# Kernel optimization log

Measured on AMD Instinct MI355X. Metric: run time of the kernel, lower is better.

The kernel has to match this reference:

```python
import jax, jax.numpy as jnp
import numpy as np

# Dimensions
B_, T_, IN_ = 8, 1024, 512          # batch, seq_len, in_dim
D_ = 1024                           # latent_dim (hidden_size)
I_ = 2048                           # intermediate_size
N_ = 64                             # state_size
H_ = 16                             # ssm_num_head
P_ = I_ // H_                       # head_dim = 128
K_ = 3                              # conv_kernel
L_ = 4                              # num_layer
OUT_, CB_ = 512, 1024               # out_dim, num_code_book
CONV_DIM = I_ + 2 * N_              # 2176
PROJ = I_ + CONV_DIM + H_           # in_proj width of mixer = 4240


def setup_inputs() -> dict:
    key = jax.random.key(0)
    ks = jax.random.split(key, 16)
    s = 0.02
    inp = {
        "x": jax.random.normal(ks[0], (B_, T_, IN_), jnp.float32),
        "in_w": jax.random.normal(ks[1], (IN_, D_), jnp.float32) * s,
        "in_b": jnp.zeros((D_,), jnp.float32),
        "norm_w": jnp.ones((L_, D_), jnp.float32),
        "mix_in_w": jax.random.normal(ks[2], (L_, D_, PROJ), jnp.float32) * s,
        "conv_w": jax.random.normal(ks[3], (L_, K_, 1, CONV_DIM), jnp.float32) * s,
        "conv_b": jnp.zeros((L_, CONV_DIM), jnp.float32),
        "dt_bias": jax.random.normal(ks[4], (L_, H_), jnp.float32) * 0.1,
        "A_log": jnp.log(jax.random.uniform(ks[5], (L_, H_), jnp.float32, 0.001, 0.1)),
        "D": jnp.ones((L_, H_), jnp.float32),
        "gnorm_w": jnp.ones((L_, I_), jnp.float32),
        "mix_out_w": jax.random.normal(ks[6], (L_, I_, D_), jnp.float32) * s,
        "out_w": jax.random.normal(ks[7], (D_, OUT_), jnp.float32) * s,
        "out_b": jnp.zeros((OUT_,), jnp.float32),
        "code_w": jax.random.normal(ks[8], (D_, CB_), jnp.float32) * s,
        "code_b": jnp.zeros((CB_,), jnp.float32),
    }
    return inp


def rmsnorm(x, w, eps=1e-6):
    v = jnp.mean(jnp.square(x), axis=-1, keepdims=True)
    return x * jax.lax.rsqrt(v + eps) * w


def mamba_block(x, nw, inw, cw, cb, dtb, alog, Dv, gnw, outw):
    residual = x
    h = rmsnorm(x, nw)
    proj = h @ inw                                   # [B,T,PROJ]
    gate, hBC, dt = jnp.split(proj, [I_, I_ + CONV_DIM], axis=-1)
    # causal depthwise conv along time
    conv = jax.lax.conv_general_dilated(
        hBC, cw, window_strides=(1,), padding=[(K_ - 1, 0)],
        dimension_numbers=("NWC", "WIO", "NWC"), feature_group_count=CONV_DIM)
    conv = jax.nn.silu(conv + cb)
    xs, Bm, Cm = jnp.split(conv, [I_, I_ + N_], axis=-1)   # [B,T,I],[B,T,N],[B,T,N]
    dt = jax.nn.softplus(dt + dtb)                   # [B,T,H]
    a = -jnp.exp(alog)                               # [H] scalar decay per head
    xh = xs.reshape(B_, T_, H_, P_)

    def step(hst, inp):
        dt_t, B_t, C_t, x_t = inp                    # [B,H],[B,N],[B,N],[B,H,P]
        dA = jnp.exp(dt_t * a)                       # [B,H]
        hst = hst * dA[:, :, None, None] + (dt_t[:, :, None, None] * x_t[..., None]) * B_t[:, None, None, :]
        y = jnp.einsum("bhpn,bn->bhp", hst, C_t)
        return hst, y

    inputs = (dt.transpose(1, 0, 2), Bm.transpose(1, 0, 2),
              Cm.transpose(1, 0, 2), xh.transpose(1, 0, 2, 3))
    h0 = jnp.zeros((B_, H_, P_, N_), x.dtype)
    _, ys = jax.lax.scan(step, h0, inputs)           # ys: [T,B,H,P]
    y = ys.transpose(1, 0, 2, 3) + Dv[None, None, :, None] * xh
    y = y.reshape(B_, T_, I_)
    y = rmsnorm(y * jax.nn.silu(gate), gnw)          # gated RMSNorm
    return residual + y @ outw


def reference(x, in_w, in_b, norm_w, mix_in_w, conv_w, conv_b, dt_bias,
              A_log, D, gnorm_w, mix_out_w, out_w, out_b, code_w, code_b):
    h = x @ in_w + in_b
    for i in range(L_):
        h = mamba_block(h, norm_w[i], mix_in_w[i], conv_w[i], conv_b[i],
                        dt_bias[i], A_log[i], D[i], gnorm_w[i], mix_out_w[i])
    return (h @ out_w + out_b, h @ code_w + code_b)
```

## Files before the change

kernel.cpp:

```cpp
#include <hip/hip_runtime.h>
#include <hip/hip_bf16.h>

typedef __hip_bfloat16 bf16;
typedef __bf16 bfv8 __attribute__((ext_vector_type(8)));
typedef float fv4 __attribute__((ext_vector_type(4)));

#define B_  8
#define T_  1024
#define INP 512
#define D_  1024
#define I_  2048
#define N_  64
#define H_  16
#define P_  128
#define L_  4
#define OUT_ 512
#define CB_ 1024
#define CONV_DIM 2176
#define PROJ 4240
#define M_  (B_*T_)
#define TC  64
#define NC  (T_/TC)

typedef const __attribute__((address_space(1))) void gv_t;
typedef __attribute__((address_space(3))) void lv_t;

__device__ __forceinline__ void load_lds16(const bf16* g, char* l) {
    __builtin_amdgcn_global_load_lds((gv_t*)g, (lv_t*)l, 16, 0, 0);
}

template <int N> __device__ __forceinline__ void wait_vm() {
    if constexpr (N == 0)      asm volatile("s_waitcnt vmcnt(0)" ::: "memory");
    else if constexpr (N == 2) asm volatile("s_waitcnt vmcnt(2)" ::: "memory");
    else if constexpr (N == 3) asm volatile("s_waitcnt vmcnt(3)" ::: "memory");
    else if constexpr (N == 4) asm volatile("s_waitcnt vmcnt(4)" ::: "memory");
    else if constexpr (N == 6) asm volatile("s_waitcnt vmcnt(6)" ::: "memory");
    else                       asm volatile("s_waitcnt vmcnt(8)" ::: "memory");
}
__device__ __forceinline__ void barrier_sync() {
    asm volatile("s_barrier" ::: "memory");
}

__global__ __launch_bounds__(256) void ingest_k(const float* __restrict__ src,
                                                bf16* __restrict__ dst, int n) {
    int i = blockIdx.x * 256 + threadIdx.x;
    if (i >= n) return;
    dst[i] = __float2bfloat16(src[i]);
}

__global__ __launch_bounds__(256) void transpose_any(const float* __restrict__ in,
                                                     size_t off,
                                                     bf16* __restrict__ out,
                                                     int R, int C) {
    __shared__ bf16 tile[32][33];
    int c0 = blockIdx.x * 32, r0 = blockIdx.y * 32;
    int tx = threadIdx.x, ty = threadIdx.y;
#pragma unroll
    for (int i = 0; i < 4; ++i) {
        int r = r0 + ty + i * 8, c = c0 + tx;
        bf16 v = __float2bfloat16(0.f);
        if (c < C) v = __float2bfloat16(in[off + (size_t)r * C + c]);
        tile[ty + i * 8][tx] = v;
    }
    __syncthreads();
#pragma unroll
    for (int i = 0; i < 4; ++i) {
        int c = c0 + ty + i * 8;
        out[(size_t)c * R + r0 + tx] = tile[tx][ty + i * 8];
    }
}

template <int MODE, int BM, int BN, int WGM, int WGN, int RING, int NTHR>
__global__ __launch_bounds__(NTHR) void gemm8p(const bf16* __restrict__ A,
                                               const bf16* __restrict__ Bt,
                                               int K, int N,
                                               const bf16* __restrict__ bias,
                                               float* __restrict__ outF,
                                               bf16* __restrict__ outB,
                                               bf16* __restrict__ outB2,
                                               float* __restrict__ outF2) {
    constexpr int HK = 32;
    constexpr int MT = BM / WGM / 16;
    constexpr int NT = BN / WGN / 16;
    constexpr int ABY = BM * HK * 2;
    constexpr int BBY = BN * HK * 2;
    constexpr int BUF = ABY + BBY;
    constexpr int RPI = NTHR / 4;
    constexpr int AL = BM / RPI;
    constexpr int BL = BN / RPI;
    constexpr int LD = AL + BL;
    constexpr int IB = NTHR * 16;

    extern __shared__ char lds[];
    const int tid = threadIdx.x;
    const int wv = tid >> 6, lane = tid & 63;
    const int l16 = lane & 15, quad = lane >> 4;
    const int wm = (wv / WGN) * (BM / WGM);
    const int wn = (wv % WGN) * (BN / WGN);

    const int NX = gridDim.x;
    const int nwg = NX * gridDim.y;
    const int orig = blockIdx.y * NX + blockIdx.x;
    const int q = nwg >> 3, r = nwg & 7, xcd = orig & 7, lid = orig >> 3;
    const int wg = (xcd < r ? xcd * (q + 1) : r * (q + 1) + (xcd - r) * q) + lid;
    const int m0 = (wg / NX) * BM;
    const int n0 = (wg % NX) * BN;

    const int srow = tid >> 2, sslot = tid & 3;
    const int swz = (sslot ^ ((srow >> 1) & 3)) << 3;
    const bf16* ga = A  + (size_t)(m0 + srow) * K + swz;
    const bf16* gb = Bt + (size_t)(n0 + srow) * K + swz;
    char* lw = lds + wv * 1024;

    const int HT = K / HK;

    auto stageA = [&](int stg, int rbuf) {
#pragma unroll
        for (int j = 0; j < AL; ++j)
            load_lds16(ga + (size_t)stg * HK + (size_t)(j * RPI) * K,
                       lw + rbuf * BUF + j * IB);
    };
    auto stageB = [&](int stg, int rbuf) {
#pragma unroll
        for (int j = 0; j < BL; ++j)
            load_lds16(gb + (size_t)stg * HK + (size_t)(j * RPI) * K,
                       lw + rbuf * BUF + ABY + j * IB);
    };

#pragma unroll
    for (int h = 0; h < RING - 1; ++h) { stageA(h, h); stageB(h, h); }
    wait_vm<LD>();
    barrier_sync();

    fv4 acc[MT][NT] = {};
    int rb = 0;
    for (int ht = 0; ht < HT; ++ht) {
        const char* Ab = lds + rb * BUF;
        const char* Bb = Ab + ABY;
        const int stg = ht + RING - 1;
        const int sb = (rb == 0) ? RING - 1 : rb - 1;
        const bool dostage = stg < HT;

        bfv8 bf[NT], af[MT];
#pragma unroll
        for (int i = 0; i < NT; ++i) {
            int rr = wn + i * 16 + l16;
            bf[i] = *(const bfv8*)(Bb + rr * 64 + ((quad ^ ((rr >> 1) & 3)) << 4));
        }
#pragma unroll
        for (int i = 0; i < MT; ++i) {
            int rr = wm + i * 16 + l16;
            af[i] = *(const bfv8*)(Ab + rr * 64 + ((quad ^ ((rr >> 1) & 3)) << 4));
        }
        if (dostage) { stageA(stg, sb); stageB(stg, sb); }
        __builtin_amdgcn_s_setprio(1);
#pragma unroll
        for (int mt = 0; mt < MT; ++mt)
#pragma unroll
            for (int nt = 0; nt < NT; ++nt)
                acc[mt][nt] = __builtin_amdgcn_mfma_f32_16x16x32_bf16(
                    af[mt], bf[nt], acc[mt][nt], 0, 0, 0);
        __builtin_amdgcn_s_setprio(0);

        int fut = HT - 1 - ht; if (fut > RING - 1) fut = RING - 1;
        if (fut >= 1) {
            int w = (fut - 1) * LD;
            if (w >= LD) wait_vm<LD>();
            else wait_vm<0>();
        }
        barrier_sync();
        rb = (rb + 1 == RING) ? 0 : rb + 1;
    }

#pragma unroll
    for (int mt = 0; mt < MT; ++mt) {
#pragma unroll
        for (int nt = 0; nt < NT; ++nt) {
#pragma unroll
            for (int i = 0; i < 4; ++i) {
                int row = m0 + wm + mt * 16 + quad * 4 + i;
                int col = n0 + wn + nt * 16 + l16;
                float v = acc[mt][nt][i];
                if (MODE == 0) {
                    v += __bfloat162float(bias[col]);
                    outF[(size_t)row * N + col] = v;
                } else if (MODE == 1) {
                    if (col < I_)
                        outB[(size_t)row * I_ + col] = __float2bfloat16(v);
                    else if (col < I_ + CONV_DIM)
                        outB2[(size_t)row * CONV_DIM + (col - I_)] = __float2bfloat16(v);
                    else if (col < PROJ)
                        outF2[(size_t)row * H_ + (col - (I_ + CONV_DIM))] = v;
                } else if (MODE == 2) {
                    outF[(size_t)row * N + col] += v;
                }
            }
        }
    }
}

__global__ __launch_bounds__(256) void rmsnorm_k(const float* __restrict__ x,
                                                 const bf16* __restrict__ w,
                                                 bf16* __restrict__ out) {
    int row = blockIdx.x, tid = threadIdx.x;
    float4 v = *(const float4*)&x[(size_t)row * D_ + tid * 4];
    float ss = v.x * v.x + v.y * v.y + v.z * v.z + v.w * v.w;
#pragma unroll
    for (int off = 32; off; off >>= 1) ss += __shfl_down(ss, off);
    __shared__ float sb[4];
    if ((tid & 63) == 0) sb[tid >> 6] = ss;
    __syncthreads();
    ss = sb[0] + sb[1] + sb[2] + sb[3];
    float rs = rsqrtf(ss * (1.f / D_) + 1e-6f);
    float xv[4] = {v.x, v.y, v.z, v.w};
#pragma unroll
    for (int j = 0; j < 4; ++j)
        out[(size_t)row * D_ + tid * 4 + j] =
            __float2bfloat16(xv[j] * rs * __bfloat162float(w[tid * 4 + j]));
}

__global__ __launch_bounds__(256) void gatednorm_k(const bf16* __restrict__ y,
                                                   const bf16* __restrict__ g,
                                                   const bf16* __restrict__ w,
                                                   bf16* __restrict__ out) {
    int row = blockIdx.x, tid = threadIdx.x;
    size_t base = (size_t)row * I_ + tid * 8;
    bf16 yv[8], gv[8];
    *(uint4*)yv = *(const uint4*)&y[base];
    *(uint4*)gv = *(const uint4*)&g[base];
    float vv[8]; float ss = 0.f;
#pragma unroll
    for (int j = 0; j < 8; ++j) {
        float yf = __bfloat162float(yv[j]);
        float gf = __bfloat162float(gv[j]);
        float sig = 1.f / (1.f + expf(-gf));
        vv[j] = yf * gf * sig;
        ss += vv[j] * vv[j];
    }
#pragma unroll
    for (int off = 32; off; off >>= 1) ss += __shfl_down(ss, off);
    __shared__ float sb[4];
    if ((tid & 63) == 0) sb[tid >> 6] = ss;
    __syncthreads();
    ss = sb[0] + sb[1] + sb[2] + sb[3];
    float rs = rsqrtf(ss * (1.f / I_) + 1e-6f);
    bf16 ov[8];
#pragma unroll
    for (int j = 0; j < 8; ++j)
        ov[j] = __float2bfloat16(vv[j] * rs * __bfloat162float(w[tid * 8 + j]));
    *(uint4*)&out[base] = *(uint4*)ov;
}

__global__ __launch_bounds__(256) void conv_k(const bf16* __restrict__ hbc,
                                              const bf16* __restrict__ w,
                                              const bf16* __restrict__ bias,
                                              bf16* __restrict__ xs,
                                              float* __restrict__ bc) {
    int cq = blockIdx.x * 256 + threadIdx.x;
    if (cq >= CONV_DIM / 4) return;
    int c = cq * 4;
    int bt = blockIdx.y;
    int t = bt & (T_ - 1);
    float acc[4];
#pragma unroll
    for (int j = 0; j < 4; ++j) acc[j] = __bfloat162float(bias[c + j]);
#pragma unroll
    for (int k = 0; k < 3; ++k) {
        int tt = t - 2 + k;
        if (tt < 0) continue;
        const bf16* src = &hbc[(size_t)(bt - 2 + k) * CONV_DIM + c];
#pragma unroll
        for (int j = 0; j < 4; ++j)
            acc[j] = fmaf(__bfloat162float(w[k * CONV_DIM + c + j]),
                          __bfloat162float(src[j]), acc[j]);
    }
#pragma unroll
    for (int j = 0; j < 4; ++j) {
        float v = acc[j];
        v = v / (1.f + expf(-v));
        if (c + j < I_) xs[(size_t)bt * I_ + c + j] = __float2bfloat16(v);
        else            bc[(size_t)bt * 128 + (c + j - I_)] = v;
    }
}

__global__ __launch_bounds__(256) void dtprep_k(const float* __restrict__ dtraw,
                                                const float* __restrict__ dtb,
                                                const float* __restrict__ alog,
                                                float* __restrict__ wco,
                                                float* __restrict__ gma) {
    int chain = blockIdx.x * 4 + (threadIdx.x >> 6);
    int s = threadIdx.x & 63;
    int h = chain & 15, ci = (chain >> 4) & (NC - 1), b = chain >> 8;
    float a = -expf(alog[h]);
    float bz = dtb[h];
    int idx = (b * T_ + ci * TC + s) * H_ + h;
    float z = dtraw[idx] + bz;
    float dt = fmaxf(z, 0.f) + log1pf(expf(-fabsf(z)));
    float ps = dt * a;
#pragma unroll
    for (int d = 1; d < 64; d <<= 1) {
        float o = __shfl_up(ps, d, 64);
        if (s >= d) ps += o;
    }
    float g = expf(ps);
    wco[idx] = dt / g;
    gma[idx] = g;
}

__global__ __launch_bounds__(128) void scan_local_k(const bf16* __restrict__ xs,
                                                    const float* __restrict__ bc,
                                                    const float* __restrict__ wco,
                                                    const float* __restrict__ gma,
                                                    const float* __restrict__ dvec,
                                                    bf16* __restrict__ yout,
                                                    bf16* __restrict__ sfin) {
    int bid = blockIdx.x;
    int ci = bid & (NC - 1);
    int h  = (bid >> 4) & (H_ - 1);
    int b  = bid >> 8;
    int p = threadIdx.x;
    float Dv = dvec[h];
    float st[64];
#pragma unroll
    for (int n = 0; n < 64; ++n) st[n] = 0.f;
    int bt0 = b * T_ + ci * TC;
    const bf16* xptr = xs + (size_t)bt0 * I_ + h * P_ + p;
    bf16* yptr = yout + (size_t)bt0 * I_ + h * P_ + p;
    float xv_n = __bfloat162float(xptr[0]);
    for (int s = 0; s < TC; ++s) {
        float xv = xv_n;
        if (s + 1 < TC) xv_n = __bfloat162float(xptr[(size_t)(s + 1) * I_]);
        float w = wco[(bt0 + s) * H_ + h];
        float g = gma[(bt0 + s) * H_ + h];
        float cc = w * xv;
        const float4* B4 = (const float4*)&bc[(size_t)(bt0 + s) * 128];
#pragma unroll
        for (int j = 0; j < 16; ++j) {
            float4 bv = B4[j];
            st[4 * j + 0] = fmaf(cc, bv.x, st[4 * j + 0]);
            st[4 * j + 1] = fmaf(cc, bv.y, st[4 * j + 1]);
            st[4 * j + 2] = fmaf(cc, bv.z, st[4 * j + 2]);
            st[4 * j + 3] = fmaf(cc, bv.w, st[4 * j + 3]);
        }
        float y0 = 0.f, y1 = 0.f, y2 = 0.f, y3 = 0.f;
#pragma unroll
        for (int j = 0; j < 16; ++j) {
            float4 cv = B4[16 + j];
            y0 = fmaf(st[4 * j + 0], cv.x, y0);
            y1 = fmaf(st[4 * j + 1], cv.y, y1);
            y2 = fmaf(st[4 * j + 2], cv.z, y2);
            y3 = fmaf(st[4 * j + 3], cv.w, y3);
        }
        yptr[(size_t)s * I_] = __float2bfloat16(fmaf(g, (y0 + y1) + (y2 + y3), Dv * xv));
    }
    float G = gma[(bt0 + TC - 1) * H_ + h];
    bf16* sf = sfin + (size_t)bid * (128 * 64);
#pragma unroll
    for (int n = 0; n < 64; ++n) sf[n * 128 + p] = __float2bfloat16(st[n] * G);
}

__global__ __launch_bounds__(128) void scan_combine_k(bf16* __restrict__ sbuf,
                                                      const float* __restrict__ gma) {
    int bid = blockIdx.x;
    int n = bid & 63;
    int h = (bid >> 6) & (H_ - 1);
    int b = bid >> 10;
    int p = threadIdx.x;
    size_t base0 = ((size_t)(b * (H_ * NC) + h * NC) * (128 * 64)) + n * 128 + p;
    int gbase = b * T_ * H_ + h;
    float S = 0.f;
#pragma unroll
    for (int ci = 0; ci < NC; ++ci) {
        bf16* addr = sbuf + base0 + (size_t)ci * (128 * 64);
        float tmp = __bfloat162float(*addr);
        *addr = __float2bfloat16(S);
        float G = gma[gbase + (ci * TC + TC - 1) * H_];
        S = fmaf(G, S, tmp);
    }
}

__global__ __launch_bounds__(128) void scan_correct_k(const bf16* __restrict__ sinit,
                                                      const float* __restrict__ gma,
                                                      const float* __restrict__ bc,
                                                      bf16* __restrict__ yout) {
    int bid = blockIdx.x;
    int ci = bid & (NC - 1);
    if (ci == 0) return;
    int h = (bid >> 4) & (H_ - 1);
    int b = bid >> 8;
    int p = threadIdx.x;
    const bf16* sb = sinit + (size_t)bid * (128 * 64);
    float S[64];
#pragma unroll
    for (int n = 0; n < 64; ++n) S[n] = __bfloat162float(sb[n * 128 + p]);
    int bt0 = b * T_ + ci * TC;
    bf16* yptr = yout + (size_t)bt0 * I_ + h * P_ + p;
    for (int s = 0; s < TC; ++s) {
        float g = gma[(bt0 + s) * H_ + h];
        const float4* C4 = (const float4*)&bc[(size_t)(bt0 + s) * 128 + 64];
        float y0 = 0.f, y1 = 0.f, y2 = 0.f, y3 = 0.f;
#pragma unroll
        for (int j = 0; j < 16; ++j) {
            float4 cv = C4[j];
            y0 = fmaf(S[4 * j + 0], cv.x, y0);
            y1 = fmaf(S[4 * j + 1], cv.y, y1);
            y2 = fmaf(S[4 * j + 2], cv.z, y2);
            y3 = fmaf(S[4 * j + 3], cv.w, y3);
        }
        float y = __bfloat162float(yptr[(size_t)s * I_]);
        yptr[(size_t)s * I_] = __float2bfloat16(fmaf(g, (y0 + y1) + (y2 + y3), y));
    }
}

__global__ __launch_bounds__(256) void cast_f2b_k(const float* __restrict__ in,
                                                  bf16* __restrict__ out) {
    int i = (blockIdx.x * 256 + threadIdx.x) * 4;
    float4 v = *(const float4*)&in[i];
    bf16 ov[4] = {__float2bfloat16(v.x), __float2bfloat16(v.y),
                  __float2bfloat16(v.z), __float2bfloat16(v.w)};
    *(uint2*)&out[i] = *(uint2*)ov;
}


static inline size_t align256(size_t x) { return (x + 255) & ~(size_t)255; }

extern "C" void kernel_launch(void* const* d_in, const int* in_sizes, int n_in,
                              void* d_out, int out_size, void* d_ws, size_t ws_size,
                              hipStream_t stream) {
    const float* x_in     = (const float*)d_in[0];
    const float* in_w     = (const float*)d_in[1];
    const float* in_b     = (const float*)d_in[2];
    const float* norm_w   = (const float*)d_in[3];
    const float* mix_in_w = (const float*)d_in[4];
    const float* conv_w   = (const float*)d_in[5];
    const float* conv_b   = (const float*)d_in[6];
    const float* dt_bias  = (const float*)d_in[7];
    const float* A_log    = (const float*)d_in[8];
    const float* Dvec     = (const float*)d_in[9];
    const float* gnorm_w  = (const float*)d_in[10];
    const float* mix_out_w= (const float*)d_in[11];
    const float* out_w    = (const float*)d_in[12];
    const float* out_b    = (const float*)d_in[13];
    const float* code_w   = (const float*)d_in[14];
    const float* code_b   = (const float*)d_in[15];
    float* outF0 = (float*)d_out;
    float* outF1 = (float*)d_out + (size_t)M_ * OUT_;

    char* p = (char*)d_ws;
    auto alloc = [&](size_t bytes) -> char* { char* r = p; p += align256(bytes); return r; };

    bf16*  xb       = (bf16*)alloc((size_t)M_ * INP * 2);
    bf16*  v_inb    = (bf16*)alloc(D_ * 2);
    bf16*  v_normw  = (bf16*)alloc(L_ * D_ * 2);
    bf16*  v_convw  = (bf16*)alloc(L_ * 3 * CONV_DIM * 2);
    bf16*  v_convb  = (bf16*)alloc(L_ * CONV_DIM * 2);
    bf16*  v_gnw    = (bf16*)alloc(L_ * I_ * 2);
    bf16*  v_outb   = (bf16*)alloc(OUT_ * 2);
    bf16*  v_codeb  = (bf16*)alloc(CB_ * 2);
    bf16*  wt_in    = (bf16*)alloc((size_t)1024 * 512 * 2);
    bf16*  wt_big   = (bf16*)alloc((size_t)4352 * 1024 * 2);
    bf16*  wt_small = (bf16*)alloc((size_t)1024 * 2048 * 2);
    bf16*  wt_out   = (bf16*)alloc((size_t)512 * 1024 * 2);
    bf16*  wt_code  = (bf16*)alloc((size_t)1024 * 1024 * 2);
    float* hbuf     = (float*)alloc((size_t)M_ * D_ * 4);
    bf16*  hn       = (bf16*)alloc((size_t)M_ * D_ * 2);
    bf16*  gate     = (bf16*)alloc((size_t)M_ * I_ * 2);
    bf16*  hbc      = (bf16*)alloc((size_t)M_ * CONV_DIM * 2);
    float* dtraw    = (float*)alloc((size_t)M_ * H_ * 4);
    bf16*  xs       = (bf16*)alloc((size_t)M_ * I_ * 2);
    float* bcbuf    = (float*)alloc((size_t)M_ * 128 * 4);
    float* wcob     = (float*)alloc((size_t)M_ * H_ * 4);
    float* gmab     = (float*)alloc((size_t)M_ * H_ * 4);
    bf16*  sfin     = (bf16*)alloc((size_t)B_ * H_ * NC * 128 * 64 * 2);
    (void)in_sizes; (void)n_in; (void)out_size;

    size_t needed = (size_t)(p - (char*)d_ws);
    if (needed > ws_size) return;

    constexpr size_t SH_PROJ = 73728;
    constexpr size_t SH_SQ   = 49152;
    static bool attr_done = false;
    if (!attr_done) {
        attr_done = true;
        (void)hipFuncSetAttribute((const void*)gemm8p<1, 256, 128, 4, 2, 3, 512>,
                                  hipFuncAttributeMaxDynamicSharedMemorySize, (int)SH_PROJ);
        (void)hipFuncSetAttribute((const void*)gemm8p<0, 128, 128, 2, 2, 3, 256>,
                                  hipFuncAttributeMaxDynamicSharedMemorySize, (int)SH_SQ);
        (void)hipFuncSetAttribute((const void*)gemm8p<2, 128, 128, 2, 2, 3, 256>,
                                  hipFuncAttributeMaxDynamicSharedMemorySize, (int)SH_SQ);
    }

    auto ing = [&](const float* src, bf16* dst, int n) {
        ingest_k<<<(n + 255) / 256, 256, 0, stream>>>(src, dst, n);
    };
    ing(x_in, xb, M_ * INP);
    ing(in_b, v_inb, D_);
    ing(norm_w, v_normw, L_ * D_);
    ing(conv_w, v_convw, L_ * 3 * CONV_DIM);
    ing(conv_b, v_convb, L_ * CONV_DIM);
    ing(gnorm_w, v_gnw, L_ * I_);
    ing(out_b, v_outb, OUT_);
    ing(code_b, v_codeb, CB_);

    dim3 tb(32, 8);
    transpose_any<<<dim3(32, 16), tb, 0, stream>>>(in_w, 0, wt_in, 512, 1024);
    transpose_any<<<dim3(16, 32), tb, 0, stream>>>(out_w, 0, wt_out, 1024, 512);
    transpose_any<<<dim3(32, 32), tb, 0, stream>>>(code_w, 0, wt_code, 1024, 1024);

    gemm8p<0, 128, 128, 2, 2, 3, 256><<<dim3(8, 64), 256, SH_SQ, stream>>>(
        xb, wt_in, INP, D_, v_inb, hbuf, nullptr, nullptr, nullptr);

    for (int i = 0; i < L_; ++i) {
        transpose_any<<<dim3(136, 32), tb, 0, stream>>>(mix_in_w, (size_t)i * 1024 * PROJ,
                                                        wt_big, 1024, PROJ);
        transpose_any<<<dim3(32, 64), tb, 0, stream>>>(mix_out_w, (size_t)i * 2048 * 1024,
                                                       wt_small, 2048, 1024);
        rmsnorm_k<<<M_, 256, 0, stream>>>(hbuf, v_normw + i * D_, hn);
        gemm8p<1, 256, 128, 4, 2, 3, 512><<<dim3(34, 32), 512, SH_PROJ, stream>>>(
            hn, wt_big, D_, 4352, nullptr, nullptr, gate, hbc, dtraw);
        conv_k<<<dim3(3, M_), 256, 0, stream>>>(hbc, v_convw + i * 3 * CONV_DIM,
                                                v_convb + i * CONV_DIM, xs, bcbuf);
        dtprep_k<<<B_ * NC * H_ / 4, 256, 0, stream>>>(
            dtraw, dt_bias + i * H_, A_log + i * H_, wcob, gmab);
        scan_local_k<<<B_ * H_ * NC, 128, 0, stream>>>(xs, bcbuf, wcob, gmab,
                                                       Dvec + i * H_, hbc, sfin);
        scan_combine_k<<<B_ * H_ * 64, 128, 0, stream>>>(sfin, gmab);
        scan_correct_k<<<B_ * H_ * NC, 128, 0, stream>>>(sfin, gmab, bcbuf, hbc);
        gatednorm_k<<<M_, 256, 0, stream>>>(hbc, gate, v_gnw + i * I_, xs);
        gemm8p<2, 128, 128, 2, 2, 3, 256><<<dim3(8, 64), 256, SH_SQ, stream>>>(
            xs, wt_small, I_, D_, nullptr, hbuf, nullptr, nullptr, nullptr);
    }

    cast_f2b_k<<<(M_ * D_) / 1024, 256, 0, stream>>>(hbuf, hn);
    gemm8p<0, 128, 128, 2, 2, 3, 256><<<dim3(4, 64), 256, SH_SQ, stream>>>(
        hn, wt_out, D_, OUT_, v_outb, outF0, nullptr, nullptr, nullptr);
    gemm8p<0, 128, 128, 2, 2, 3, 256><<<dim3(8, 64), 256, SH_SQ, stream>>>(
        hn, wt_code, D_, CB_, v_codeb, outF1, nullptr, nullptr, nullptr);
}
```

Before: 1.902 ms.

## Reformulate chunked SSM scan as MFMA matrix products (SSD-style)

Replaces the per-thread sequential intra-chunk scan and state-correction kernels with an SSD-style chunked formulation. Each wave builds the masked decay-weighted C·Bᵀ matrix in LDS, multiplies it against the chunk's x to get y, and computes the chunk-final state as x·(scaled B)ᵀ, all on bf16 MFMA. The inter-chunk correction also becomes an MFMA C·S product. Two new transpose kernels lay out x and B time-major-contiguous for the MFMA operands, and the xt buffer shares memory with hn/xb. This adds bf16 rounding of intermediate products and extra transpose traffic in exchange for moving the serial scalar FMA loops onto matrix units.

```diff
diff --git a/kernel.cpp b/kernel.cpp
--- a/kernel.cpp
+++ b/kernel.cpp
@@ -39,6 +39,28 @@
 }
 __device__ __forceinline__ void barrier_sync() {
     asm volatile("s_barrier" ::: "memory");
+}
+
+__device__ __forceinline__ fv4 MF(bfv8 a, bfv8 b, fv4 c) {
+    return __builtin_amdgcn_mfma_f32_16x16x32_bf16(a, b, c, 0, 0, 0);
+}
+__device__ __forceinline__ __bf16 f2b(float x) {
+    __hip_bfloat16 h = __float2bfloat16(x);
+    union { unsigned short u; __bf16 b; } t;
+    t.u = *reinterpret_cast<unsigned short*>(&h);
+    return t.b;
+}
+__device__ __forceinline__ float bb2f(__bf16 x) {
+    union { __bf16 b; unsigned short u; } t; t.b = x;
+    union { unsigned int u; float f; } r; r.u = (unsigned int)t.u << 16;
+    return r.f;
+}
+__device__ __forceinline__ bfv8 cvt8f(const float* p) {
+    float4 a = *(const float4*)p, b = *(const float4*)(p + 4);
+    bfv8 r;
+    r[0] = f2b(a.x); r[1] = f2b(a.y); r[2] = f2b(a.z); r[3] = f2b(a.w);
+    r[4] = f2b(b.x); r[5] = f2b(b.y); r[6] = f2b(b.z); r[7] = f2b(b.w);
+    return r;
 }
 
 __global__ __launch_bounds__(256) void ingest_k(const float* __restrict__ src,
@@ -158,8 +180,7 @@
         for (int mt = 0; mt < MT; ++mt)
 #pragma unroll
             for (int nt = 0; nt < NT; ++nt)
-                acc[mt][nt] = __builtin_amdgcn_mfma_f32_16x16x32_bf16(
-                    af[mt], bf[nt], acc[mt][nt], 0, 0, 0);
+                acc[mt][nt] = MF(af[mt], bf[nt], acc[mt][nt]);
         __builtin_amdgcn_s_setprio(0);
 
         int fut = HT - 1 - ht; if (fut > RING - 1) fut = RING - 1;
@@ -307,56 +328,190 @@
     gma[idx] = g;
 }
 
-__global__ __launch_bounds__(128) void scan_local_k(const bf16* __restrict__ xs,
-                                                    const float* __restrict__ bc,
-                                                    const float* __restrict__ wco,
-                                                    const float* __restrict__ gma,
-                                                    const float* __restrict__ dvec,
-                                                    bf16* __restrict__ yout,
-                                                    bf16* __restrict__ sfin) {
-    int bid = blockIdx.x;
-    int ci = bid & (NC - 1);
-    int h  = (bid >> 4) & (H_ - 1);
-    int b  = bid >> 8;
-    int p = threadIdx.x;
+__global__ __launch_bounds__(256) void xpose_k(const bf16* __restrict__ in,
+                                               bf16* __restrict__ out) {
+    __shared__ bf16 tl[64][72];
+    int t0 = blockIdx.x * 64;
+    int by = blockIdx.y;
+    int pg = by & 1, h = (by >> 1) & 15, b = by >> 5;
+    int p0 = pg * 64;
+    int tx = threadIdx.x & 15, ty = threadIdx.x >> 4;
+#pragma unroll
+    for (int i = 0; i < 4; ++i) {
+        ushort4 v = *(const ushort4*)&in[(size_t)(b * T_ + t0 + ty + 16 * i) * 2048
+                                         + h * 128 + p0 + tx * 4];
+        tl[ty + 16 * i][tx * 4 + 0] = *(bf16*)&v.x;
+        tl[ty + 16 * i][tx * 4 + 1] = *(bf16*)&v.y;
+        tl[ty + 16 * i][tx * 4 + 2] = *(bf16*)&v.z;
+        tl[ty + 16 * i][tx * 4 + 3] = *(bf16*)&v.w;
+    }
+    __syncthreads();
+#pragma unroll
+    for (int i = 0; i < 4; ++i) {
+        ushort4 v;
+        v.x = *(unsigned short*)&tl[tx * 4 + 0][ty + 16 * i];
+        v.y = *(unsigned short*)&tl[tx * 4 + 1][ty + 16 * i];
+        v.z = *(unsigned short*)&tl[tx * 4 + 2][ty + 16 * i];
+        v.w = *(unsigned short*)&tl[tx * 4 + 3][ty + 16 * i];
+        *(ushort4*)&out[(size_t)((b * 16 + h) * 128 + p0 + ty + 16 * i) * 1024
+                        + t0 + tx * 4] = v;
+    }
+}
+
+__global__ __launch_bounds__(256) void btpose_k(const float* __restrict__ in,
+                                                bf16* __restrict__ out) {
+    __shared__ bf16 tl[64][72];
+    int t0 = blockIdx.x * 64;
+    int b = blockIdx.y;
+    int tx = threadIdx.x & 15, ty = threadIdx.x >> 4;
+#pragma unroll
+    for (int i = 0; i < 4; ++i) {
+        float4 v = *(const float4*)&in[(size_t)(b * T_ + t0 + ty + 16 * i) * 128 + tx * 4];
+        tl[ty + 16 * i][tx * 4 + 0] = __float2bfloat16(v.x);
+        tl[ty + 16 * i][tx * 4 + 1] = __float2bfloat16(v.y);
+        tl[ty + 16 * i][tx * 4 + 2] = __float2bfloat16(v.z);
+        tl[ty + 16 * i][tx * 4 + 3] = __float2bfloat16(v.w);
+    }
+    __syncthreads();
+#pragma unroll
+    for (int i = 0; i < 4; ++i) {
+        ushort4 v;
+        v.x = *(unsigned short*)&tl[tx * 4 + 0][ty + 16 * i];
+        v.y = *(unsigned short*)&tl[tx * 4 + 1][ty + 16 * i];
+        v.z = *(unsigned short*)&tl[tx * 4 + 2][ty + 16 * i];
+        v.w = *(unsigned short*)&tl[tx * 4 + 3][ty + 16 * i];
+        *(ushort4*)&out[(size_t)(b * 64 + ty + 16 * i) * 1024 + t0 + tx * 4] = v;
+    }
+}
+
+__global__ __launch_bounds__(256) void scan_mm_k(const float* __restrict__ bc,
+                                                 const bf16* __restrict__ xt,
+                                                 const bf16* __restrict__ btb,
+                                                 const float* __restrict__ wco,
+                                                 const float* __restrict__ gma,
+                                                 const float* __restrict__ dvec,
+                                                 const bf16* __restrict__ xs,
+                                                 bf16* __restrict__ yout,
+                                                 bf16* __restrict__ sfin) {
+    __shared__ __align__(64) char plds[4][8192];
+    const int wv = threadIdx.x >> 6, lane = threadIdx.x & 63;
+    const int l16 = lane & 15, quad = lane >> 4;
+    const int wid = blockIdx.x * 4 + wv;
+    const int ci = wid & (NC - 1), h = (wid >> 4) & (H_ - 1), b = wid >> 8;
+    const int bt0 = b * T_ + ci * TC;
+    char* Pb = plds[wv];
+
+    float wl = wco[(size_t)(bt0 + lane) * H_ + h];
+    float gl = gma[(size_t)(bt0 + lane) * H_ + h];
+    float g63 = __shfl(gl, 63);
     float Dv = dvec[h];
-    float st[64];
-#pragma unroll
-    for (int n = 0; n < 64; ++n) st[n] = 0.f;
-    int bt0 = b * T_ + ci * TC;
-    const bf16* xptr = xs + (size_t)bt0 * I_ + h * P_ + p;
-    bf16* yptr = yout + (size_t)bt0 * I_ + h * P_ + p;
-    float xv_n = __bfloat162float(xptr[0]);
-    for (int s = 0; s < TC; ++s) {
-        float xv = xv_n;
-        if (s + 1 < TC) xv_n = __bfloat162float(xptr[(size_t)(s + 1) * I_]);
-        float w = wco[(bt0 + s) * H_ + h];
-        float g = gma[(bt0 + s) * H_ + h];
-        float cc = w * xv;
-        const float4* B4 = (const float4*)&bc[(size_t)(bt0 + s) * 128];
-#pragma unroll
-        for (int j = 0; j < 16; ++j) {
-            float4 bv = B4[j];
-            st[4 * j + 0] = fmaf(cc, bv.x, st[4 * j + 0]);
-            st[4 * j + 1] = fmaf(cc, bv.y, st[4 * j + 1]);
-            st[4 * j + 2] = fmaf(cc, bv.z, st[4 * j + 2]);
-            st[4 * j + 3] = fmaf(cc, bv.w, st[4 * j + 3]);
-        }
-        float y0 = 0.f, y1 = 0.f, y2 = 0.f, y3 = 0.f;
-#pragma unroll
-        for (int j = 0; j < 16; ++j) {
-            float4 cv = B4[16 + j];
-            y0 = fmaf(st[4 * j + 0], cv.x, y0);
-            y1 = fmaf(st[4 * j + 1], cv.y, y1);
-            y2 = fmaf(st[4 * j + 2], cv.z, y2);
-            y3 = fmaf(st[4 * j + 3], cv.w, y3);
-        }
-        yptr[(size_t)s * I_] = __float2bfloat16(fmaf(g, (y0 + y1) + (y2 + y3), Dv * xv));
-    }
-    float G = gma[(bt0 + TC - 1) * H_ + h];
-    bf16* sf = sfin + (size_t)bid * (128 * 64);
-#pragma unroll
-    for (int n = 0; n < 64; ++n) sf[n * 128 + p] = __float2bfloat16(st[n] * G);
+
+    float wsv[4], gmv[4][4];
+#pragma unroll
+    for (int s4 = 0; s4 < 4; ++s4) wsv[s4] = __shfl(wl, s4 * 16 + l16);
+#pragma unroll
+    for (int t4 = 0; t4 < 4; ++t4)
+#pragma unroll
+        for (int i = 0; i < 4; ++i) gmv[t4][i] = __shfl(gl, t4 * 16 + quad * 4 + i);
+
+    fv4 g[4][4] = {};
+#pragma unroll
+    for (int kq = 0; kq < 2; ++kq) {
+        bfv8 cf[4], bfr[4];
+#pragma unroll
+        for (int i = 0; i < 4; ++i) {
+            cf[i]  = cvt8f(&bc[(size_t)(bt0 + i * 16 + l16) * 128 + 64 + kq * 32 + quad * 8]);
+            bfr[i] = cvt8f(&bc[(size_t)(bt0 + i * 16 + l16) * 128 + kq * 32 + quad * 8]);
+        }
+#pragma unroll
+        for (int t4 = 0; t4 < 4; ++t4)
+#pragma unroll
+            for (int s4 = 0; s4 < 4; ++s4)
+                g[t4][s4] = MF(cf[t4], bfr[s4], g[t4][s4]);
+    }
+
+#pragma unroll
+    for (int t4 = 0; t4 < 4; ++t4)
+#pragma unroll
+        for (int s4 = 0; s4 < 4; ++s4)
+#pragma unroll
+            for (int i = 0; i < 4; ++i) {
+                int t = t4 * 16 + quad * 4 + i, s = s4 * 16 + l16;
+                float pv = (s <= t) ? g[t4][s4][i] * gmv[t4][i] * wsv[s4] : 0.f;
+                int slot = (s >> 3) ^ (t & 7);
+                *(__bf16*)(Pb + t * 128 + slot * 16 + (s & 7) * 2) = f2b(pv);
+            }
+
+    bfv8 xf[8][2];
+    const bf16* xtp = xt + (size_t)((b * 16 + h) * 128) * 1024 + ci * 64;
+#pragma unroll
+    for (int p4 = 0; p4 < 8; ++p4)
+#pragma unroll
+        for (int kq = 0; kq < 2; ++kq)
+            xf[p4][kq] = *(const bfv8*)&xtp[(size_t)(p4 * 16 + l16) * 1024 + kq * 32 + quad * 8];
+
+    fv4 y[4][8] = {};
+#pragma unroll
+    for (int t4 = 0; t4 < 4; ++t4) {
+#pragma unroll
+        for (int kq = 0; kq < ((t4 < 2) ? 1 : 2); ++kq) {
+            int rr = t4 * 16 + l16;
+            bfv8 pf = *(const bfv8*)(Pb + rr * 128 + (((kq * 4 + quad) ^ (rr & 7)) << 4));
+#pragma unroll
+            for (int p4 = 0; p4 < 8; ++p4)
+                y[t4][p4] = MF(pf, xf[p4][kq], y[t4][p4]);
+        }
+    }
+
+    bf16* yp = yout + (size_t)bt0 * I_ + h * P_;
+    const bf16* xp = xs + (size_t)bt0 * I_ + h * P_;
+#pragma unroll
+    for (int t4 = 0; t4 < 4; ++t4)
+#pragma unroll
+        for (int p4 = 0; p4 < 8; ++p4)
+#pragma unroll
+            for (int i = 0; i < 4; ++i) {
+                size_t a = (size_t)(t4 * 16 + quad * 4 + i) * I_ + p4 * 16 + l16;
+                float xv = __bfloat162float(xp[a]);
+                yp[a] = __float2bfloat16(y[t4][p4][i] + Dv * xv);
+            }
+
+    float ws8[2][8];
+#pragma unroll
+    for (int kq = 0; kq < 2; ++kq)
+#pragma unroll
+        for (int j = 0; j < 8; ++j)
+            ws8[kq][j] = g63 * __shfl(wl, kq * 32 + quad * 8 + j);
+
+    fv4 sa[8][4] = {};
+    const bf16* btp = btb + (size_t)b * 64 * 1024 + ci * 64;
+#pragma unroll
+    for (int kq = 0; kq < 2; ++kq) {
+        bfv8 sbv[4];
+#pragma unroll
+        for (int n4 = 0; n4 < 4; ++n4) {
+            bfv8 raw = *(const bfv8*)&btp[(size_t)(n4 * 16 + l16) * 1024 + kq * 32 + quad * 8];
+            bfv8 sb;
+#pragma unroll
+            for (int j = 0; j < 8; ++j) sb[j] = f2b(bb2f(raw[j]) * ws8[kq][j]);
+            sbv[n4] = sb;
+        }
+#pragma unroll
+        for (int p4 = 0; p4 < 8; ++p4)
+#pragma unroll
+            for (int n4 = 0; n4 < 4; ++n4)
+                sa[p4][n4] = MF(xf[p4][kq], sbv[n4], sa[p4][n4]);
+    }
+
+    bf16* sp = sfin + (size_t)wid * (128 * 64);
+#pragma unroll
+    for (int p4 = 0; p4 < 8; ++p4)
+#pragma unroll
+        for (int n4 = 0; n4 < 4; ++n4)
+#pragma unroll
+            for (int i = 0; i < 4; ++i)
+                sp[(p4 * 16 + quad * 4 + i) * 64 + n4 * 16 + l16] =
+                    __float2bfloat16(sa[p4][n4][i]);
 }
 
 __global__ __launch_bounds__(128) void scan_combine_k(bf16* __restrict__ sbuf,
@@ -379,37 +534,54 @@
     }
 }
 
-__global__ __launch_bounds__(128) void scan_correct_k(const bf16* __restrict__ sinit,
-                                                      const float* __restrict__ gma,
-                                                      const float* __restrict__ bc,
-                                                      bf16* __restrict__ yout) {
-    int bid = blockIdx.x;
-    int ci = bid & (NC - 1);
+__global__ __launch_bounds__(256) void scan_corr_k(const float* __restrict__ bc,
+                                                   const bf16* __restrict__ sfin,
+                                                   const float* __restrict__ gma,
+                                                   bf16* __restrict__ yout) {
+    const int wv = threadIdx.x >> 6, lane = threadIdx.x & 63;
+    const int wid = blockIdx.x * 4 + wv;
+    const int ci = wid & (NC - 1), h = (wid >> 4) & (H_ - 1), b = wid >> 8;
     if (ci == 0) return;
-    int h = (bid >> 4) & (H_ - 1);
-    int b = bid >> 8;
-    int p = threadIdx.x;
-    const bf16* sb = sinit + (size_t)bid * (128 * 64);
-    float S[64];
-#pragma unroll
-    for (int n = 0; n < 64; ++n) S[n] = __bfloat162float(sb[n * 128 + p]);
-    int bt0 = b * T_ + ci * TC;
-    bf16* yptr = yout + (size_t)bt0 * I_ + h * P_ + p;
-    for (int s = 0; s < TC; ++s) {
-        float g = gma[(bt0 + s) * H_ + h];
-        const float4* C4 = (const float4*)&bc[(size_t)(bt0 + s) * 128 + 64];
-        float y0 = 0.f, y1 = 0.f, y2 = 0.f, y3 = 0.f;
-#pragma unroll
-        for (int j = 0; j < 16; ++j) {
-            float4 cv = C4[j];
-            y0 = fmaf(S[4 * j + 0], cv.x, y0);
-            y1 = fmaf(S[4 * j + 1], cv.y, y1);
-            y2 = fmaf(S[4 * j + 2], cv.z, y2);
-            y3 = fmaf(S[4 * j + 3], cv.w, y3);
-        }
-        float y = __bfloat162float(yptr[(size_t)s * I_]);
-        yptr[(size_t)s * I_] = __float2bfloat16(fmaf(g, (y0 + y1) + (y2 + y3), y));
-    }
+    const int l16 = lane & 15, quad = lane >> 4;
+    const int bt0 = b * T_ + ci * TC;
+
+    float gl = gma[(size_t)(bt0 + lane) * H_ + h];
+    float gmv[4][4];
+#pragma unroll
+    for (int t4 = 0; t4 < 4; ++t4)
+#pragma unroll
+        for (int i = 0; i < 4; ++i) gmv[t4][i] = __shfl(gl, t4 * 16 + quad * 4 + i);
+
+    const bf16* sp = sfin + (size_t)wid * (128 * 64);
+    fv4 z[4][8] = {};
+#pragma unroll
+    for (int kq = 0; kq < 2; ++kq) {
+        bfv8 cf[4];
+#pragma unroll
+        for (int i = 0; i < 4; ++i)
+            cf[i] = cvt8f(&bc[(size_t)(bt0 + i * 16 + l16) * 128 + 64 + kq * 32 + quad * 8]);
+#pragma unroll
+        for (int p4 = 0; p4 < 8; ++p4) {
+            bfv8 sf = *(const bfv8*)&sp[(p4 * 16 + l16) * 64 + kq * 32 + quad * 8];
+#pragma unroll
+            for (int t4 = 0; t4 < 4; ++t4)
+                z[t4][p4] = MF(cf[t4], sf, z[t4][p4]);
+        }
+    }
+
+    bf16* yp = yout + (size_t)bt0 * I_ + h * P_;
+#pragma unroll
+    for (int t4 = 0; t4 < 4; ++t4)
+#pragma unroll
+        for (int i = 0; i < 4; ++i) {
+            float gm = gmv[t4][i];
+#pragma unroll
+            for (int p4 = 0; p4 < 8; ++p4) {
+                size_t a = (size_t)(t4 * 16 + quad * 4 + i) * I_ + p4 * 16 + l16;
+                float yv = __bfloat162float(yp[a]);
+                yp[a] = __float2bfloat16(yv + gm * z[t4][p4][i]);
+            }
+        }
 }
 
 __global__ __launch_bounds__(256) void cast_f2b_k(const float* __restrict__ in,
@@ -449,7 +621,9 @@
     char* p = (char*)d_ws;
     auto alloc = [&](size_t bytes) -> char* { char* r = p; p += align256(bytes); return r; };
 
-    bf16*  xb       = (bf16*)alloc((size_t)M_ * INP * 2);
+    bf16*  xt       = (bf16*)alloc((size_t)B_ * H_ * 128 * T_ * 2);
+    bf16*  hn       = xt;
+    bf16*  xb       = xt + (size_t)M_ * D_;
     bf16*  v_inb    = (bf16*)alloc(D_ * 2);
     bf16*  v_normw  = (bf16*)alloc(L_ * D_ * 2);
     bf16*  v_convw  = (bf16*)alloc(L_ * 3 * CONV_DIM * 2);
@@ -463,7 +637,6 @@
     bf16*  wt_out   = (bf16*)alloc((size_t)512 * 1024 * 2);
     bf16*  wt_code  = (bf16*)alloc((size_t)1024 * 1024 * 2);
     float* hbuf     = (float*)alloc((size_t)M_ * D_ * 4);
-    bf16*  hn       = (bf16*)alloc((size_t)M_ * D_ * 2);
     bf16*  gate     = (bf16*)alloc((size_t)M_ * I_ * 2);
     bf16*  hbc      = (bf16*)alloc((size_t)M_ * CONV_DIM * 2);
     float* dtraw    = (float*)alloc((size_t)M_ * H_ * 4);
@@ -472,6 +645,7 @@
     float* wcob     = (float*)alloc((size_t)M_ * H_ * 4);
     float* gmab     = (float*)alloc((size_t)M_ * H_ * 4);
     bf16*  sfin     = (bf16*)alloc((size_t)B_ * H_ * NC * 128 * 64 * 2);
+    bf16*  bt16     = (bf16*)alloc((size_t)B_ * 64 * T_ * 2);
     (void)in_sizes; (void)n_in; (void)out_size;
 
     size_t needed = (size_t)(p - (char*)d_ws);
@@ -522,10 +696,12 @@
                                                 v_convb + i * CONV_DIM, xs, bcbuf);
         dtprep_k<<<B_ * NC * H_ / 4, 256, 0, stream>>>(
             dtraw, dt_bias + i * H_, A_log + i * H_, wcob, gmab);
-        scan_local_k<<<B_ * H_ * NC, 128, 0, stream>>>(xs, bcbuf, wcob, gmab,
-                                                       Dvec + i * H_, hbc, sfin);
+        xpose_k<<<dim3(16, 256), 256, 0, stream>>>(xs, xt);
+        btpose_k<<<dim3(16, 8), 256, 0, stream>>>(bcbuf, bt16);
+        scan_mm_k<<<512, 256, 0, stream>>>(bcbuf, xt, bt16, wcob, gmab,
+                                           Dvec + i * H_, xs, hbc, sfin);
         scan_combine_k<<<B_ * H_ * 64, 128, 0, stream>>>(sfin, gmab);
-        scan_correct_k<<<B_ * H_ * NC, 128, 0, stream>>>(sfin, gmab, bcbuf, hbc);
+        scan_corr_k<<<512, 256, 0, stream>>>(bcbuf, sfin, gmab, hbc);
         gatednorm_k<<<M_, 256, 0, stream>>>(hbc, gate, v_gnw + i * I_, xs);
         gemm8p<2, 128, 128, 2, 2, 3, 256><<<dim3(8, 64), 256, SH_SQ, stream>>>(
             xs, wt_small, I_, D_, nullptr, hbuf, nullptr, nullptr, nullptr);
```

New measurement: 1.647 ms. -13.4%, faster.
